# Kernel tuning notes

Measured on AMD Instinct MI355X. Metric: run time of the kernel, lower is better.

The kernel has to match this reference:

```python
import jax, jax.numpy as jnp
import numpy as np

B = 64        # graphs
N0 = 2048     # nodes per graph
DEG = 16      # avg degree
IN = 128      # input_dim
H = 30        # hcs
NH = 11       # heads
OD = 8        # output_dim[i]
K1, K2, K3 = 1844, 1660, 1494  # ceil(0.9*n) chain


def setup_inputs() -> dict:
    key = jax.random.key(0)
    ks = jax.random.split(key, 32)
    N = B * N0
    E = N * DEG
    x = jax.random.normal(ks[0], (N, IN), jnp.float32)
    g = jnp.repeat(jnp.arange(B, dtype=jnp.int32), N0 * DEG)
    src = g * N0 + jax.random.randint(ks[1], (E,), 0, N0, dtype=jnp.int32)
    dst = g * N0 + jax.random.randint(ks[2], (E,), 0, N0, dtype=jnp.int32)
    edge_index = jnp.stack([src, dst])
    edge_attr = jax.random.uniform(ks[3], (E,), jnp.float32)
    batch = jnp.repeat(jnp.arange(B, dtype=jnp.int32), N0)
    s = 0.05
    def W(k, *shape):
        return jax.random.normal(k, shape, jnp.float32) * s
    return {
        'x': x, 'edge_index': edge_index, 'edge_attr': edge_attr, 'batch': batch,
        'ln_g': jnp.ones((IN,), jnp.float32), 'ln_b': jnp.zeros((IN,), jnp.float32),
        'W_rel1': W(ks[4], IN, H), 'b_rel1': W(ks[5], H), 'W_root1': W(ks[6], IN, H),
        'W_rel2': W(ks[7], H, H), 'b_rel2': W(ks[8], H), 'W_root2': W(ks[9], H, H),
        'W_rel3': W(ks[10], H, H), 'b_rel3': W(ks[11], H), 'W_root3': W(ks[12], H, H),
        'pool_w1': W(ks[13], H), 'pool_w2': W(ks[14], H), 'pool_w3': W(ks[15], H),
        'head_W1': W(ks[16], NH, 2 * H, 8 * H), 'head_b1': W(ks[17], NH, 8 * H),
        'head_W2': W(ks[18], NH, 8 * H, 32 * H), 'head_b2': W(ks[19], NH, 32 * H),
        'head_W3': W(ks[20], NH, 32 * H, OD), 'head_b3': W(ks[21], NH, OD),
    }


def _layernorm(x, g, b):
    m = x.mean(-1, keepdims=True)
    v = ((x - m) ** 2).mean(-1, keepdims=True)
    return (x - m) * jax.lax.rsqrt(v + 1e-5) * g + b


def _gconv(x, src, dst, ew, Wr, br, Ws, N):
    # PyG GraphConv: out = lin_rel(sum_j ew*x_j) + lin_root(x)
    agg = jax.ops.segment_sum(x[src] * ew[:, None], dst, num_segments=N)
    return agg @ Wr + br + x @ Ws


def _topk_pool(x, src, dst, ew, w, n, k):
    # score = tanh(x.w/||w||); keep top-k per graph; gate kept nodes by score
    score = jnp.tanh((x @ w) / jnp.linalg.norm(w)).reshape(B, n)
    vals, idx = jax.lax.top_k(score, k)                      # [B,k]
    xg = x.reshape(B, n, -1)
    xk = jnp.take_along_axis(xg, idx[:, :, None], axis=1) * vals[:, :, None]
    x_new = xk.reshape(B * k, -1)
    newidx = jnp.full((B, n), -1, jnp.int32)
    newidx = newidx.at[jnp.arange(B)[:, None], idx].set(
        jnp.broadcast_to(jnp.arange(k, dtype=jnp.int32), (B, k)))
    g = src // n
    ns = newidx[g, src % n]
    nd = newidx[g, dst % n]
    keep = (ns >= 0) & (nd >= 0)
    src_new = jnp.where(keep, g * k + ns, 0)
    dst_new = jnp.where(keep, g * k + nd, 0)
    ew_new = jnp.where(keep, ew, 0.0)
    return x_new, src_new, dst_new, ew_new


def _readout(x, k):
    xg = x.reshape(B, k, -1)
    return jnp.concatenate([xg.max(axis=1), xg.mean(axis=1)], axis=1)  # [B,2H]


def reference(x, edge_index, edge_attr, batch, ln_g, ln_b,
              W_rel1, b_rel1, W_root1, W_rel2, b_rel2, W_root2,
              W_rel3, b_rel3, W_root3, pool_w1, pool_w2, pool_w3,
              head_W1, head_b1, head_W2, head_b2, head_W3, head_b3):
    src, dst = edge_index[0], edge_index[1]
    ew = edge_attr
    h = _layernorm(x, ln_g, ln_b)

    h = jax.nn.relu(_gconv(h, src, dst, ew, W_rel1, b_rel1, W_root1, B * N0))
    h, src, dst, ew = _topk_pool(h, src, dst, ew, pool_w1, N0, K1)
    x1 = _readout(h, K1)

    h = jax.nn.relu(_gconv(h, src, dst, ew, W_rel2, b_rel2, W_root2, B * K1))
    h, src, dst, ew = _topk_pool(h, src, dst, ew, pool_w2, K1, K2)
    x2 = _readout(h, K2)

    h = jax.nn.relu(_gconv(h, src, dst, ew, W_rel3, b_rel3, W_root3, B * K2))
    h, src, dst, ew = _topk_pool(h, src, dst, ew, pool_w3, K2, K3)
    x3 = _readout(h, K3)

    z = jax.nn.relu(x1 + x2 + x3)                                   # [B,60]
    a = jax.nn.relu(jnp.einsum('bd,hdo->hbo', z, head_W1) + head_b1[:, None, :])
    a = jax.nn.relu(jnp.einsum('hbo,hop->hbp', a, head_W2) + head_b2[:, None, :])
    out = jnp.einsum('hbp,hpq->hbq', a, head_W3) + head_b3[:, None, :]
    return out  # [11, B, 8]
```

## Files before the change

kernel.cpp:

```cpp
#include <hip/hip_runtime.h>
#include <hip/hip_bf16.h>

#define B 64
#define N0 2048
#define DEG 16
#define IN_DIM 128
#define H 30
#define NH 11
#define K1 1844
#define K2 1660
#define K3 1494
#define NTOT (B * N0)
#define ETOT (NTOT * DEG)
#define RSTRIDE 32
#define RT 64
#define ESTRIDE1 32768
#define RSEG 16

__global__ __launch_bounds__(256) void k_prep(
    const float* __restrict__ ln_g, const float* __restrict__ ln_b,
    const float* __restrict__ Wrel1, const float* __restrict__ brel1, const float* __restrict__ Wroot1,
    const float* __restrict__ Wrel2, const float* __restrict__ Wroot2,
    const float* __restrict__ Wrel3, const float* __restrict__ Wroot3,
    float* __restrict__ Wc1, float* __restrict__ S1, float* __restrict__ T1,
    float* __restrict__ Wc2, float* __restrict__ Wc3)
{
    int tid = threadIdx.x;
    for (int i = tid; i < IN_DIM * 60; i += 256) {
        int j = i / 60, c = i - j * 60;
        float w = (c < H) ? Wrel1[j * H + c] : Wroot1[j * H + (c - H)];
        Wc1[i] = w * ln_g[j];
    }
    if (tid < 60) {
        int c = tid;
        float s = 0.f, tt = 0.f;
        for (int j = 0; j < IN_DIM; ++j) {
            float w = (c < H) ? Wrel1[j * H + c] : Wroot1[j * H + (c - H)];
            s += w * ln_g[j];
            tt += w * ln_b[j];
        }
        S1[c] = s;
        T1[c] = (c < H) ? tt : tt + brel1[c - H];
    }
    for (int i = tid; i < H * 60; i += 256) {
        int j = i / 60, c = i - j * 60;
        Wc2[i] = (c < H) ? Wrel2[j * H + c] : Wroot2[j * H + (c - H)];
        Wc3[i] = (c < H) ? Wrel3[j * H + c] : Wroot3[j * H + (c - H)];
    }
}

__global__ __launch_bounds__(256) void k_lnproj(
    const float* __restrict__ x, const float* __restrict__ Wc,
    const float* __restrict__ S, const float* __restrict__ T,
    float* __restrict__ rt)
{
    int cg = blockIdx.y;
    int row = blockIdx.x * 256 + threadIdx.x;
    const float4* xr4 = (const float4*)(x + (size_t)row * IN_DIM);
    const float* wbase = Wc + cg * 15;
    float acc[15];
#pragma unroll
    for (int c = 0; c < 15; ++c) acc[c] = 0.f;
    float sum = 0.f, sumsq = 0.f;
    for (int k4 = 0; k4 < 32; ++k4) {
        float4 xq = xr4[k4];
        float xs[4] = {xq.x, xq.y, xq.z, xq.w};
#pragma unroll
        for (int u = 0; u < 4; ++u) {
            float xv = xs[u];
            sum += xv; sumsq += xv * xv;
            const float* wrow = wbase + (k4 * 4 + u) * 60;
#pragma unroll
            for (int c = 0; c < 15; ++c) acc[c] += xv * wrow[c];
        }
    }
    float mean = sum * (1.f / 128.f);
    float var = sumsq * (1.f / 128.f) - mean * mean;
    float rstd = 1.0f / sqrtf(var + 1e-5f);
    int scol = cg * 15;
    int coff = (cg < 2) ? cg * 15 : 32 + (cg - 2) * 15;
    float* op = rt + (size_t)row * RT + coff;
#pragma unroll
    for (int c = 0; c < 15; ++c)
        op[c] = rstd * (acc[c] - mean * S[scol + c]) + T[scol + c];
}

__global__ __launch_bounds__(256) void k_proj30p(
    const float* __restrict__ hbuf, const int* __restrict__ sidx,
    const float* __restrict__ score, const float* __restrict__ Wc,
    const float* __restrict__ brel, float* __restrict__ rt,
    int n_old, int k)
{
    int cg = blockIdx.y;
    int row = blockIdx.x * 256 + threadIdx.x;
    int g = row / k, j = row - g * k;
    int idx = sidx[g * k + j];
    float val = score[g * n_old + idx];
    const float* hr = hbuf + (size_t)(g * n_old + idx) * RSTRIDE;
    const float4* hr4 = (const float4*)hr;
    const float* wbase = Wc + cg * 15;
    float acc[15];
#pragma unroll
    for (int c = 0; c < 15; ++c) acc[c] = 0.f;
#pragma unroll
    for (int m4 = 0; m4 < 7; ++m4) {
        float4 hq = hr4[m4];
        float xs[4] = {hq.x, hq.y, hq.z, hq.w};
#pragma unroll
        for (int u = 0; u < 4; ++u) {
            float xv = xs[u];
            const float* wrow = wbase + (m4 * 4 + u) * 60;
#pragma unroll
            for (int c = 0; c < 15; ++c) acc[c] += xv * wrow[c];
        }
    }
    {
        float2 h2 = *(const float2*)(hr + 28);
        const float* w28 = wbase + 28 * 60;
        const float* w29 = wbase + 29 * 60;
#pragma unroll
        for (int c = 0; c < 15; ++c)
            acc[c] += h2.x * w28[c] + h2.y * w29[c];
    }
    bool isR = (cg < 2);
    int coff = isR ? cg * 15 : 32 + (cg - 2) * 15;
    float* op = rt + (size_t)row * RT + coff;
#pragma unroll
    for (int c = 0; c < 15; ++c) {
        float bv = isR ? 0.f : brel[(cg - 2) * 15 + c];
        op[c] = val * acc[c] + bv;
    }
}

__global__ __launch_bounds__(1024) void k_hist1(
    const int* __restrict__ dst, unsigned short* __restrict__ rank,
    int* __restrict__ chunkCnt)
{
    __shared__ unsigned int cnt[2048];
    int chunk = blockIdx.x, g = chunk >> 2;
    for (int i = threadIdx.x; i < 2048; i += 1024) cnt[i] = 0;
    __syncthreads();
    int e0 = chunk * 8192;
#pragma unroll
    for (int u = 0; u < 8; ++u) {
        int e = e0 + u * 1024 + threadIdx.x;
        int d = dst[e] - g * N0;
        rank[e] = (unsigned short)atomicAdd(&cnt[d], 1u);
    }
    __syncthreads();
    for (int i = threadIdx.x; i < 2048; i += 1024) chunkCnt[chunk * 2048 + i] = cnt[i];
}

__global__ __launch_bounds__(1024) void k_scan(
    int* __restrict__ chunkCnt, int* __restrict__ runStart, int* __restrict__ runLen)
{
    __shared__ int bufA[2048], bufB[2048];
    int g = blockIdx.x;
    int c0[2], c1[2], c2[2], tt[2];
    for (int h2 = 0; h2 < 2; ++h2) {
        int d = threadIdx.x + h2 * 1024;
        c0[h2] = chunkCnt[(g * 4 + 0) * 2048 + d];
        c1[h2] = chunkCnt[(g * 4 + 1) * 2048 + d];
        c2[h2] = chunkCnt[(g * 4 + 2) * 2048 + d];
        int c3 = chunkCnt[(g * 4 + 3) * 2048 + d];
        tt[h2] = c0[h2] + c1[h2] + c2[h2] + c3;
        bufA[d] = tt[h2];
    }
    __syncthreads();
    int* s_ = bufA; int* d_ = bufB;
    for (int off = 1; off < 2048; off <<= 1) {
        for (int h2 = 0; h2 < 2; ++h2) {
            int d = threadIdx.x + h2 * 1024;
            int v = s_[d];
            if (d >= off) v += s_[d - off];
            d_[d] = v;
        }
        __syncthreads();
        int* tmp = s_; s_ = d_; d_ = tmp;
    }
    for (int h2 = 0; h2 < 2; ++h2) {
        int d = threadIdx.x + h2 * 1024;
        int ex = s_[d] - tt[h2];
        runStart[g * 2048 + d] = ex;
        runLen[g * 2048 + d] = tt[h2];
        chunkCnt[(g * 4 + 0) * 2048 + d] = ex;
        chunkCnt[(g * 4 + 1) * 2048 + d] = ex + c0[h2];
        chunkCnt[(g * 4 + 2) * 2048 + d] = ex + c0[h2] + c1[h2];
        chunkCnt[(g * 4 + 3) * 2048 + d] = ex + c0[h2] + c1[h2] + c2[h2];
    }
}

__global__ __launch_bounds__(1024) void k_scat1(
    const int* __restrict__ src, const int* __restrict__ dst, const float* __restrict__ ew,
    const unsigned short* __restrict__ rank, const int* __restrict__ chunkOff,
    float2* __restrict__ sOut)
{
    int chunk = blockIdx.x, g = chunk >> 2;
    int e0 = chunk * 8192;
#pragma unroll
    for (int u = 0; u < 8; ++u) {
        int e = e0 + u * 1024 + threadIdx.x;
        int d = dst[e] - g * N0;
        int pos = chunkOff[chunk * 2048 + d] + (int)rank[e];
        sOut[(size_t)g * ESTRIDE1 + pos] = make_float2(__int_as_float(src[e]), ew[e]);
    }
}

template<int LVL>
__global__ __launch_bounds__(256) void k_gather(
    const float2* __restrict__ sE, const int* __restrict__ runS, const int* __restrict__ runL,
    const int* __restrict__ ind1, const int* __restrict__ ind2, const int* __restrict__ mapc,
    const float* __restrict__ rt, float* __restrict__ h,
    const float* __restrict__ poolw, float* __restrict__ score,
    int n, int rK, int nblocks)
{
    int b = blockIdx.x;
    int cpx = nblocks >> 3;
    b = (b & 7) * cpx + (b >> 3);
    int slot = threadIdx.x >> 5, j = threadIdx.x & 31;
    int v = b * 8 + slot;
    int g = v / n;
    int local = v - g * n;
    int v1 = local;
    if (LVL >= 2) v1 = ind2[g * K2 + v1];
    if (LVL >= 1) v1 = ind1[g * K1 + v1];
    int s0 = runS[g * 2048 + v1], len = runL[g * 2048 + v1];
    const float2* meta = sE + (size_t)g * ESTRIDE1 + s0;
    int rbase = g * rK;
    float acc = 0.f;
    for (int c = 0; c < len; c += 8) {
        int lim = len - c; if (lim > 8) lim = 8;
        float2 m[8];
#pragma unroll
        for (int u = 0; u < 8; ++u) m[u] = meta[c + (u < lim ? u : 0)];
        int rowv[8]; float wv[8];
#pragma unroll
        for (int u = 0; u < 8; ++u) {
            int srcg = __float_as_int(m[u].x);
            float w = (u < lim) ? m[u].y : 0.f;
            if (LVL == 0) {
                rowv[u] = srcg;
            } else {
                int ss = mapc[srcg];
                rowv[u] = rbase + (ss < 0 ? 0 : ss);
                w = (ss < 0) ? 0.f : w;
            }
            wv[u] = w;
        }
#pragma unroll
        for (int u = 0; u < 8; ++u)
            acc += rt[(size_t)rowv[u] * RT + j] * wv[u];
    }
    float wj = (j < H) ? poolw[j] : 0.f;
    float hval = 0.f;
    if (j < H) {
        hval = fmaxf(acc + rt[(size_t)v * RT + 32 + j], 0.f);
        h[(size_t)v * RSTRIDE + j] = hval;
    }
    float p = hval * wj, q = wj * wj;
#pragma unroll
    for (int off = 16; off > 0; off >>= 1) {
        p += __shfl_xor(p, off, 32);
        q += __shfl_xor(q, off, 32);
    }
    if (j == 0) score[v] = tanhf(p / sqrtf(q));
}

__global__ __launch_bounds__(1024) void k_topk_map(
    const float* __restrict__ score, int* __restrict__ sidx, int* __restrict__ mapc,
    int n, int k, int first)
{
    __shared__ unsigned long long keys[2048];
    __shared__ int inv[2048];
    int g = blockIdx.x;
    for (int i = threadIdx.x; i < 2048; i += 1024) {
        unsigned long long key = ~0ull;
        if (i < n) {
            float s = score[g * n + i];
            if (s == 0.f) s = 0.f;
            unsigned u = __float_as_uint(s);
            unsigned asc = (u & 0x80000000u) ? ~u : (u | 0x80000000u);
            unsigned desc = ~asc;
            key = ((unsigned long long)desc << 32) | (unsigned)i;
        }
        keys[i] = key;
        inv[i] = -1;
    }
    __syncthreads();
    for (int kk = 2; kk <= 2048; kk <<= 1) {
        for (int jj = kk >> 1; jj > 0; jj >>= 1) {
            for (int i = threadIdx.x; i < 2048; i += 1024) {
                int ixj = i ^ jj;
                if (ixj > i) {
                    unsigned long long a = keys[i], bb = keys[ixj];
                    bool up = ((i & kk) == 0);
                    if ((a > bb) == up) { keys[i] = bb; keys[ixj] = a; }
                }
            }
            __syncthreads();
        }
    }
    for (int j = threadIdx.x; j < k; j += 1024) {
        int idx = (int)(keys[j] & 0xffffffffu);
        sidx[g * k + j] = idx;
        inv[idx] = j;
    }
    __syncthreads();
    if (first) {
        for (int v = threadIdx.x; v < N0; v += 1024)
            mapc[g * N0 + v] = inv[v];
    } else {
        for (int v = threadIdx.x; v < N0; v += 1024) {
            int m = mapc[g * N0 + v];
            mapc[g * N0 + v] = (m >= 0) ? inv[m] : -1;
        }
    }
}

__global__ __launch_bounds__(256) void k_rpart(
    const float* __restrict__ hbuf, const int* __restrict__ sidx,
    const float* __restrict__ score, float* __restrict__ pmax, float* __restrict__ psum,
    int n_old, int k)
{
    __shared__ float smax[8][32], ssum[8][32];
    int g = blockIdx.y, seg = blockIdx.x;
    int clen = (k + RSEG - 1) / RSEG;
    int start = seg * clen;
    int end = start + clen; if (end > k) end = k;
    int f = threadIdx.x & 31, rr = threadIdx.x >> 5;
    float mx = -INFINITY, sm = 0.f;
    if (f < H) {
        for (int j = start + rr; j < end; j += 8) {
            int idx = sidx[g * k + j];
            float val = score[g * n_old + idx];
            float v = hbuf[(size_t)(g * n_old + idx) * RSTRIDE + f] * val;
            mx = fmaxf(mx, v);
            sm += v;
        }
    }
    smax[rr][f] = mx; ssum[rr][f] = sm;
    __syncthreads();
    if (rr == 0) {
        for (int q = 1; q < 8; ++q) { mx = fmaxf(mx, smax[q][f]); sm += ssum[q][f]; }
        pmax[(g * RSEG + seg) * 32 + f] = mx;
        psum[(g * RSEG + seg) * 32 + f] = sm;
    }
}

__global__ __launch_bounds__(64) void k_zfin(
    const float* __restrict__ pm1, const float* __restrict__ ps1,
    const float* __restrict__ pm2, const float* __restrict__ ps2,
    const float* __restrict__ pm3, const float* __restrict__ ps3,
    float* __restrict__ z)
{
    int g = blockIdx.x, c = threadIdx.x;
    if (c >= 60) return;
    float v1, v2, v3;
    if (c < H) {
        float m1 = -INFINITY, m2 = -INFINITY, m3 = -INFINITY;
        for (int s = 0; s < RSEG; ++s) {
            m1 = fmaxf(m1, pm1[(g * RSEG + s) * 32 + c]);
            m2 = fmaxf(m2, pm2[(g * RSEG + s) * 32 + c]);
            m3 = fmaxf(m3, pm3[(g * RSEG + s) * 32 + c]);
        }
        v1 = m1; v2 = m2; v3 = m3;
    } else {
        int f = c - H;
        float s1 = 0.f, s2 = 0.f, s3 = 0.f;
        for (int s = 0; s < RSEG; ++s) {
            s1 += ps1[(g * RSEG + s) * 32 + f];
            s2 += ps2[(g * RSEG + s) * 32 + f];
            s3 += ps3[(g * RSEG + s) * 32 + f];
        }
        v1 = s1 / (float)K1; v2 = s2 / (float)K2; v3 = s3 / (float)K3;
    }
    z[g * 60 + c] = fmaxf(v1 + v2 + v3, 0.f);
}

__global__ __launch_bounds__(256) void k_mlp1(
    const float* __restrict__ z, const float* __restrict__ W,
    const float* __restrict__ bias, float* __restrict__ a)
{
    int hb = blockIdx.x, hh = hb >> 6, b = hb & 63;
    __shared__ float zr[60];
    if (threadIdx.x < 60) zr[threadIdx.x] = z[b * 60 + threadIdx.x];
    __syncthreads();
    int o = threadIdx.x;
    if (o < 240) {
        float acc = bias[hh * 240 + o];
        const float* Wp = W + hh * 60 * 240;
#pragma unroll
        for (int d = 0; d < 60; ++d) acc += zr[d] * Wp[d * 240 + o];
        a[(hh * B + b) * 240 + o] = fmaxf(acc, 0.f);
    }
}

__global__ __launch_bounds__(256) void k_mlp2(
    const float* __restrict__ a1, const float* __restrict__ W,
    const float* __restrict__ bias, float* __restrict__ a2)
{
    __shared__ float a1t[64 * 240];
    int hh = blockIdx.x / 15, ct = blockIdx.x % 15;
    const float4* ag = (const float4*)(a1 + (size_t)hh * B * 240);
    for (int i = threadIdx.x; i < 64 * 240 / 4; i += 256)
        ((float4*)a1t)[i] = ag[i];
    __syncthreads();
    int col = threadIdx.x & 63, rg = threadIdx.x >> 6;
    const float* Wp = W + (size_t)hh * 240 * 960 + ct * 64 + col;
    float acc[16];
#pragma unroll
    for (int i = 0; i < 16; ++i) acc[i] = 0.f;
#pragma unroll 4
    for (int o = 0; o < 240; ++o) {
        float w = Wp[(size_t)o * 960];
        const float* ar = &a1t[0];
#pragma unroll
        for (int i = 0; i < 16; ++i)
            acc[i] += w * ar[(rg * 16 + i) * 240 + o];
    }
    float bv = bias[hh * 960 + ct * 64 + col];
#pragma unroll
    for (int i = 0; i < 16; ++i)
        a2[((size_t)hh * B + rg * 16 + i) * 960 + ct * 64 + col] =
            fmaxf(acc[i] + bv, 0.f);
}

__global__ __launch_bounds__(64) void k_mlp3(
    const float* __restrict__ a2, const float* __restrict__ W,
    const float* __restrict__ bias, float* __restrict__ out)
{
    int hb = blockIdx.x, hh = hb >> 6, b = hb & 63;
    __shared__ float ar[960];
    __shared__ float part[64];
    for (int i = threadIdx.x; i < 960; i += 64) ar[i] = a2[(hh * B + b) * 960 + i];
    __syncthreads();
    int q = threadIdx.x & 7, c = threadIdx.x >> 3;
    const float* Wp = W + hh * 960 * 8;
    float acc = 0.f;
    for (int p = c; p < 960; p += 8) acc += ar[p] * Wp[p * 8 + q];
    part[threadIdx.x] = acc;
    __syncthreads();
    if (threadIdx.x < 8) {
        float s = bias[hh * 8 + threadIdx.x];
        for (int cc = 0; cc < 8; ++cc) s += part[cc * 8 + threadIdx.x];
        out[(hh * B + b) * 8 + threadIdx.x] = s;
    }
}

extern "C" void kernel_launch(void* const* d_in, const int* in_sizes, int n_in,
                              void* d_out, int out_size, void* d_ws, size_t ws_size,
                              hipStream_t stream)
{
    const float* x       = (const float*)d_in[0];
    const int*   eidx    = (const int*)d_in[1];
    const int*   src0    = eidx;
    const int*   dst0    = eidx + ETOT;
    const float* ew0     = (const float*)d_in[2];
    const float* ln_g    = (const float*)d_in[4];
    const float* ln_b    = (const float*)d_in[5];
    const float* W_rel1  = (const float*)d_in[6];
    const float* b_rel1  = (const float*)d_in[7];
    const float* W_root1 = (const float*)d_in[8];
    const float* W_rel2  = (const float*)d_in[9];
    const float* b_rel2  = (const float*)d_in[10];
    const float* W_root2 = (const float*)d_in[11];
    const float* W_rel3  = (const float*)d_in[12];
    const float* b_rel3  = (const float*)d_in[13];
    const float* W_root3 = (const float*)d_in[14];
    const float* pool_w1 = (const float*)d_in[15];
    const float* pool_w2 = (const float*)d_in[16];
    const float* pool_w3 = (const float*)d_in[17];
    const float* head_W1 = (const float*)d_in[18];
    const float* head_b1 = (const float*)d_in[19];
    const float* head_W2 = (const float*)d_in[20];
    const float* head_b2 = (const float*)d_in[21];
    const float* head_W3 = (const float*)d_in[22];
    const float* head_b3 = (const float*)d_in[23];

    float* ws     = (float*)d_ws;
    float* rtbuf  = ws;
    float* abuf   = rtbuf + (size_t)NTOT * RT;
    float2* sA    = (float2*)(abuf + (size_t)NTOT * RSTRIDE);
    float* score  = (float*)(sA + (size_t)B * ESTRIDE1);
    int*   sidxA  = (int*)(score + NTOT);
    int*   sidxB  = sidxA + B * K1;
    int*   sidxC  = sidxB + B * K2;
    int*   mapc   = sidxC + B * K3;
    int*   runSA  = mapc + NTOT;
    int*   runLA  = runSA + B * 2048;
    float* pm1    = (float*)(runLA + B * 2048);
    float* ps1    = pm1 + B * RSEG * 32;
    float* pm2    = ps1 + B * RSEG * 32;
    float* ps2    = pm2 + B * RSEG * 32;
    float* pm3    = ps2 + B * RSEG * 32;
    float* ps3    = pm3 + B * RSEG * 32;
    float* zb     = ps3 + B * RSEG * 32;
    float* Wc1    = zb + B * 60;
    float* S1     = Wc1 + IN_DIM * 60;
    float* T1     = S1 + 60;
    float* Wc2    = T1 + 60;
    float* Wc3    = Wc2 + H * 60;
    int* chunkBuf         = (int*)abuf;
    unsigned short* rank  = (unsigned short*)((char*)abuf + (4u << 20));
    float* a1 = rtbuf;
    float* a2 = a1 + NH * B * 240;

    k_prep<<<1, 256, 0, stream>>>(ln_g, ln_b, W_rel1, b_rel1, W_root1,
                                  W_rel2, W_root2, W_rel3, W_root3,
                                  Wc1, S1, T1, Wc2, Wc3);

    k_hist1<<<256, 1024, 0, stream>>>(dst0, rank, chunkBuf);
    k_scan<<<B, 1024, 0, stream>>>(chunkBuf, runSA, runLA);
    k_scat1<<<256, 1024, 0, stream>>>(src0, dst0, ew0, rank, chunkBuf, sA);

    k_lnproj<<<dim3(NTOT / 256, 4), 256, 0, stream>>>(x, Wc1, S1, T1, rtbuf);
    k_gather<0><<<NTOT / 8, 256, 0, stream>>>(sA, runSA, runLA, nullptr, nullptr, nullptr,
                                              rtbuf, abuf, pool_w1, score,
                                              N0, N0, NTOT / 8);
    k_topk_map<<<B, 1024, 0, stream>>>(score, sidxA, mapc, N0, K1, 1);
    k_rpart<<<dim3(RSEG, B), 256, 0, stream>>>(abuf, sidxA, score, pm1, ps1, N0, K1);
    k_proj30p<<<dim3(B * K1 / 256, 4), 256, 0, stream>>>(abuf, sidxA, score, Wc2, b_rel2,
                                                         rtbuf, N0, K1);

    k_gather<1><<<B * K1 / 8, 256, 0, stream>>>(sA, runSA, runLA, sidxA, nullptr, mapc,
                                                rtbuf, abuf, pool_w2, score,
                                                K1, K1, B * K1 / 8);
    k_topk_map<<<B, 1024, 0, stream>>>(score, sidxB, mapc, K1, K2, 0);
    k_rpart<<<dim3(RSEG, B), 256, 0, stream>>>(abuf, sidxB, score, pm2, ps2, K1, K2);
    k_proj30p<<<dim3(B * K2 / 256, 4), 256, 0, stream>>>(abuf, sidxB, score, Wc3, b_rel3,
                                                         rtbuf, K1, K2);

    k_gather<2><<<B * K2 / 8, 256, 0, stream>>>(sA, runSA, runLA, sidxA, sidxB, mapc,
                                                rtbuf, abuf, pool_w3, score,
                                                K2, K2, B * K2 / 8);
    k_topk_map<<<B, 1024, 0, stream>>>(score, sidxC, mapc, K2, K3, 0);
    k_rpart<<<dim3(RSEG, B), 256, 0, stream>>>(abuf, sidxC, score, pm3, ps3, K2, K3);

    k_zfin<<<B, 64, 0, stream>>>(pm1, ps1, pm2, ps2, pm3, ps3, zb);
    k_mlp1<<<NH * B, 256, 0, stream>>>(zb, head_W1, head_b1, a1);
    k_mlp2<<<NH * 15, 256, 0, stream>>>(a1, head_W2, head_b2, a2);
    k_mlp3<<<NH * B, 64, 0, stream>>>(a2, head_W3, head_b3, (float*)d_out);
}
```

Measured before the change: 674.0 us.

## Split projection output into four 16-wide column planes with float4 stores

The projection kernels previously wrote 15-column groups into an interleaved 64-float row, using scalar stores at misaligned offsets. They now write each column group to its own plane of 16 floats per row, padded, using four float4 stores. The aggregation gather reads from the rel planes with a 64-byte stride instead of 256 bytes, so each gathered row touches fewer cache lines. In exchange, each half-warp reads a separate plane, and the lanes at index 30 and above duplicate reads of column 14.

```diff
diff --git a/kernel.cpp b/kernel.cpp
--- a/kernel.cpp
+++ b/kernel.cpp
@@ -13,7 +13,6 @@
 #define NTOT (B * N0)
 #define ETOT (NTOT * DEG)
 #define RSTRIDE 32
-#define RT 64
 #define ESTRIDE1 32768
 #define RSEG 16
 
@@ -78,11 +77,16 @@
     float var = sumsq * (1.f / 128.f) - mean * mean;
     float rstd = 1.0f / sqrtf(var + 1e-5f);
     int scol = cg * 15;
-    int coff = (cg < 2) ? cg * 15 : 32 + (cg - 2) * 15;
-    float* op = rt + (size_t)row * RT + coff;
+    float o[16];
 #pragma unroll
     for (int c = 0; c < 15; ++c)
-        op[c] = rstd * (acc[c] - mean * S[scol + c]) + T[scol + c];
+        o[c] = rstd * (acc[c] - mean * S[scol + c]) + T[scol + c];
+    o[15] = 0.f;
+    float4* op = (float4*)(rt + ((size_t)cg * NTOT + row) * 16);
+    op[0] = make_float4(o[0], o[1], o[2], o[3]);
+    op[1] = make_float4(o[4], o[5], o[6], o[7]);
+    op[2] = make_float4(o[8], o[9], o[10], o[11]);
+    op[3] = make_float4(o[12], o[13], o[14], o[15]);
 }
 
 __global__ __launch_bounds__(256) void k_proj30p(
@@ -123,13 +127,18 @@
             acc[c] += h2.x * w28[c] + h2.y * w29[c];
     }
     bool isR = (cg < 2);
-    int coff = isR ? cg * 15 : 32 + (cg - 2) * 15;
-    float* op = rt + (size_t)row * RT + coff;
+    float o[16];
 #pragma unroll
     for (int c = 0; c < 15; ++c) {
         float bv = isR ? 0.f : brel[(cg - 2) * 15 + c];
-        op[c] = val * acc[c] + bv;
-    }
+        o[c] = val * acc[c] + bv;
+    }
+    o[15] = 0.f;
+    float4* op = (float4*)(rt + ((size_t)cg * NTOT + row) * 16);
+    op[0] = make_float4(o[0], o[1], o[2], o[3]);
+    op[1] = make_float4(o[4], o[5], o[6], o[7]);
+    op[2] = make_float4(o[8], o[9], o[10], o[11]);
+    op[3] = make_float4(o[12], o[13], o[14], o[15]);
 }
 
 __global__ __launch_bounds__(1024) void k_hist1(
@@ -227,6 +236,8 @@
     int s0 = runS[g * 2048 + v1], len = runL[g * 2048 + v1];
     const float2* meta = sE + (size_t)g * ESTRIDE1 + s0;
     int rbase = g * rK;
+    int oj = (j < 15) ? j : ((j < 30) ? j - 15 : 14);
+    const float* rplane = rt + ((j < 15) ? 0 : ((size_t)NTOT * 16)) + oj;
     float acc = 0.f;
     for (int c = 0; c < len; c += 8) {
         int lim = len - c; if (lim > 8) lim = 8;
@@ -249,12 +260,13 @@
         }
 #pragma unroll
         for (int u = 0; u < 8; ++u)
-            acc += rt[(size_t)rowv[u] * RT + j] * wv[u];
+            acc += rplane[(size_t)rowv[u] * 16] * wv[u];
     }
     float wj = (j < H) ? poolw[j] : 0.f;
     float hval = 0.f;
     if (j < H) {
-        hval = fmaxf(acc + rt[(size_t)v * RT + 32 + j], 0.f);
+        size_t tp = (j < 15) ? 2 : 3;
+        hval = fmaxf(acc + rt[(tp * NTOT + v) * 16 + oj], 0.f);
         h[(size_t)v * RSTRIDE + j] = hval;
     }
     float p = hval * wj, q = wj * wj;
@@ -479,7 +491,7 @@
 
     float* ws     = (float*)d_ws;
     float* rtbuf  = ws;
-    float* abuf   = rtbuf + (size_t)NTOT * RT;
+    float* abuf   = rtbuf + (size_t)NTOT * 64;
     float2* sA    = (float2*)(abuf + (size_t)NTOT * RSTRIDE);
     float* score  = (float*)(sA + (size_t)B * ESTRIDE1);
     int*   sidxA  = (int*)(score + NTOT);
```

New measurement: 605.3 us. 1.11x faster.
